# Optimization experiments

Hardware: AMD Instinct MI355X
Metric: run time of the kernel (lower is better)

## Reference

```python
import jax, jax.numpy as jnp
import numpy as np
import math

EMBED_DIM = 512
NUM_HEADS = 8
HEAD_DIM = EMBED_DIM // NUM_HEADS
B, S = 1, 4096


def setup_inputs() -> dict:
    key = jax.random.key(0)
    ks = jax.random.split(key, 9)
    scale = 1.0 / math.sqrt(EMBED_DIM)
    x = jax.random.normal(ks[0], (B, S, EMBED_DIM), dtype=jnp.float32)
    # causal mask, broadcastable to (B, H, S, S); 0 => masked
    mask = jnp.tril(jnp.ones((S, S), dtype=bool))[None, None, :, :]
    Wq = jax.random.normal(ks[1], (EMBED_DIM, EMBED_DIM), jnp.float32) * scale
    bq = jnp.zeros((EMBED_DIM,), jnp.float32)
    Wk = jax.random.normal(ks[2], (EMBED_DIM, EMBED_DIM), jnp.float32) * scale
    bk = jnp.zeros((EMBED_DIM,), jnp.float32)
    Wv = jax.random.normal(ks[3], (EMBED_DIM, EMBED_DIM), jnp.float32) * scale
    bv = jnp.zeros((EMBED_DIM,), jnp.float32)
    Wo = jax.random.normal(ks[4], (EMBED_DIM, EMBED_DIM), jnp.float32) * scale
    bo = jnp.zeros((EMBED_DIM,), jnp.float32)
    return {"x": x, "mask": mask, "Wq": Wq, "bq": bq, "Wk": Wk, "bk": bk,
            "Wv": Wv, "bv": bv, "Wo": Wo, "bo": bo}


def reference(x, mask, Wq, bq, Wk, bk, Wv, bv, Wo, bo):
    Bz, Sz, E = x.shape
    H, D = NUM_HEADS, HEAD_DIM
    qk_scale = math.sqrt(D)
    # linear projections then split heads: (B, S, E) -> (B, H, S, D)
    q = (x @ Wq + bq).reshape(Bz, Sz, H, D).transpose(0, 2, 1, 3)
    k = (x @ Wk + bk).reshape(Bz, Sz, H, D).transpose(0, 2, 1, 3)
    v = (x @ Wv + bv).reshape(Bz, Sz, H, D).transpose(0, 2, 1, 3)
    # naive full score matrix (B, H, S, S) as in the original module
    scores = jnp.einsum('bhqd,bhkd->bhqk', q, k) / qk_scale
    scores = jnp.where(mask, scores, jnp.float32(-jnp.inf))
    attn_weights = jax.nn.softmax(scores, axis=-1)
    attn_output = jnp.einsum('bhqk,bhkd->bhqd', attn_weights, v)
    attn_output = attn_output.transpose(0, 2, 1, 3).reshape(Bz, Sz, E)
    output = attn_output @ Wo + bo
    return output, attn_weights
```

## Files before the change

kernel.cpp:

```cpp
#include <hip/hip_runtime.h>

typedef unsigned short u16;
typedef __attribute__((ext_vector_type(8))) _Float16 f16x8;
typedef __attribute__((ext_vector_type(4))) float f32x4;

#define S 4096
#define E 512
#define NH 8
#define HD 64
#define NG 8
#define KBG 8

__device__ __forceinline__ u16 f2h(float f) {
  union { _Float16 h; u16 u; } v; v.h = (_Float16)f; return v.u;
}

__global__ void xfrag_kernel(const float* __restrict__ x, u16* __restrict__ XF) {
  int o = blockIdx.x * blockDim.x + threadIdx.x;
  int l = o & 63, ks = (o >> 6) & 15, w = (o >> 10) & 3, mb = o >> 12;
  int row = mb * 64 + w * 16 + (l & 15);
  int col = ks * 32 + ((l >> 4) << 3);
  const float4 f0 = *(const float4*)&x[row * 512 + col];
  const float4 f1 = *(const float4*)&x[row * 512 + col + 4];
  f16x8 v;
  v[0] = (_Float16)f0.x; v[1] = (_Float16)f0.y; v[2] = (_Float16)f0.z; v[3] = (_Float16)f0.w;
  v[4] = (_Float16)f1.x; v[5] = (_Float16)f1.y; v[6] = (_Float16)f1.z; v[7] = (_Float16)f1.w;
  *(f16x8*)&XF[o * 8] = v;
}

__global__ void wfrag_kernel(const float* __restrict__ Wq, const float* __restrict__ Wk,
                             const float* __restrict__ Wv, const float* __restrict__ Wo,
                             u16* __restrict__ wqF, u16* __restrict__ wkF,
                             u16* __restrict__ wvF, u16* __restrict__ woF) {
  int o = blockIdx.x * blockDim.x + threadIdx.x;
  int which = blockIdx.y;
  int l = o & 63, ks = (o >> 6) & 15, ct = (o >> 10) & 3, nb = o >> 12;
  int n = nb * 64 + ct * 16 + (l & 15);
  int k0 = ks * 32 + ((l >> 4) << 3);
  const float* W = which == 0 ? Wq : which == 1 ? Wk : which == 2 ? Wv : Wo;
  u16* dst = which == 0 ? wqF : which == 1 ? wkF : which == 2 ? wvF : woF;
  f16x8 v;
#pragma unroll
  for (int j = 0; j < 8; ++j) v[j] = (_Float16)W[(k0 + j) * 512 + n];
  *(f16x8*)&dst[o * 8] = v;
}

template <int MODE>
__global__ __launch_bounds__(256) void gemm_kernel(
    const u16* __restrict__ AF, const u16* __restrict__ BF,
    const float* __restrict__ bias, float premul,
    u16* __restrict__ outh, float* __restrict__ outf) {
  const int mb = blockIdx.x, nb = blockIdx.y;
  const int w = threadIdx.x >> 6, l = threadIdx.x & 63;
  const int lr = l & 15, hi4 = l >> 4;

  f32x4 acc[4] = {{0.f,0.f,0.f,0.f},{0.f,0.f,0.f,0.f},{0.f,0.f,0.f,0.f},{0.f,0.f,0.f,0.f}};

  const u16* abase = AF + (size_t)((mb * 4 + w) * 16) * 512 + l * 8;
  const u16* bbase = BF + (size_t)(nb * 4 * 16) * 512 + l * 8;
#pragma unroll
  for (int ks = 0; ks < 16; ++ks) {
    f16x8 ah = *(const f16x8*)(abase + ks * 512);
#pragma unroll
    for (int ct = 0; ct < 4; ++ct) {
      f16x8 bh = *(const f16x8*)(bbase + (ct * 16 + ks) * 512);
      acc[ct] = __builtin_amdgcn_mfma_f32_16x16x32_f16(ah, bh, acc[ct], 0, 0, 0);
    }
  }

  if constexpr (MODE == 3) {
    __shared__ __align__(16) float sm[4][16][68];
#pragma unroll
    for (int ct = 0; ct < 4; ++ct) {
      float bia = bias[nb * 64 + ct * 16 + lr];
#pragma unroll
      for (int r = 0; r < 4; ++r)
        sm[w][hi4 * 4 + r][ct * 16 + lr] = (acc[ct][r] + bia) * premul;
    }
    asm volatile("s_waitcnt lgkmcnt(0)" ::: "memory");
#pragma unroll
    for (int half = 0; half < 2; ++half) {
      const float* src = &sm[w][lr][half * 32 + hi4 * 8];
      const f32x4 f0 = *(const f32x4*)src;
      const f32x4 f1 = *(const f32x4*)(src + 4);
      f16x8 o8;
      o8[0] = (_Float16)f0[0]; o8[1] = (_Float16)f0[1];
      o8[2] = (_Float16)f0[2]; o8[3] = (_Float16)f0[3];
      o8[4] = (_Float16)f1[0]; o8[5] = (_Float16)f1[1];
      o8[6] = (_Float16)f1[2]; o8[7] = (_Float16)f1[3];
      *(f16x8*)&outh[(size_t)(nb * 64 + mb) * 4096 + w * 1024 + half * 512 + l * 8] = o8;
    }
  } else {
    const int rb = mb * 64 + w * 16 + hi4 * 4;
#pragma unroll
    for (int ct = 0; ct < 4; ++ct) {
      int n = nb * 64 + ct * 16 + lr;
      float bia = bias[n];
#pragma unroll
      for (int r = 0; r < 4; ++r) {
        float v = acc[ct][r] + bia;
        if constexpr (MODE == 0) {
          outh[(rb + r) * E + n] = f2h(v);
        } else {
          outf[(rb + r) * E + n] = v;
        }
      }
    }
  }
}

__global__ void repackV_kernel(const u16* __restrict__ V, u16* __restrict__ VF) {
  int o = blockIdx.x * blockDim.x + threadIdx.x;
  int l = o & 63, half = (o >> 6) & 1, ct = (o >> 7) & 3, kb = (o >> 9) & 63, h = o >> 15;
  int col = h * 64 + ct * 16 + (l & 15);
  int row0 = kb * 64 + half * 32 + ((l >> 4) << 3);
  f16x8 v;
#pragma unroll
  for (int j = 0; j < 8; ++j)
    v[j] = *(const _Float16*)&V[(row0 + j) * 512 + col];
  *(f16x8*)&VF[o * 8] = v;
}

__global__ __launch_bounds__(256) void ksum_kernel(
    const u16* __restrict__ QF, const u16* __restrict__ KF,
    float* __restrict__ ws_l, float* __restrict__ attw) {
  const int gx = blockIdx.x;
  const int h = blockIdx.y;
  const int qb = 63 - (int)blockIdx.z;
  const int kb0 = gx * KBG;
  const int t = threadIdx.x;
  if (kb0 > qb) {
    const size_t base = (size_t)(h * S + qb * 64) * S + gx * 512;
    const f32x4 z = {0.f, 0.f, 0.f, 0.f};
#pragma unroll
    for (int j = 0; j < 32; ++j) {
      int idx = j * 256 + t;
      int row = idx >> 7, c4 = idx & 127;
      __builtin_nontemporal_store(z, (f32x4*)&attw[base + (size_t)row * S + c4 * 4]);
    }
    return;
  }
  const int w = t >> 6, l = t & 63;
  const int lr = l & 15, hi4 = l >> 4;
  const int q0 = qb * 64;

  const int qbase = (h * 64 + qb) * 4096 + w * 1024 + l * 8;
  f16x8 q0f = *(const f16x8*)&QF[qbase];
  f16x8 q1f = *(const f16x8*)&QF[qbase + 512];

  const int rowg = q0 + w * 16 + hi4 * 4;
  float acc[4] = {0.f, 0.f, 0.f, 0.f};

  const int kbend = min(kb0 + KBG, qb + 1);
  for (int kb = kb0; kb < kbend; ++kb) {
    const int kbase = (h * 64 + kb) * 4096 + l * 8;
#pragma unroll
    for (int ct = 0; ct < 4; ++ct) {
      f16x8 k0 = *(const f16x8*)&KF[kbase + ct * 1024];
      f16x8 k1 = *(const f16x8*)&KF[kbase + ct * 1024 + 512];
      f32x4 a = {0.f, 0.f, 0.f, 0.f};
      a = __builtin_amdgcn_mfma_f32_16x16x32_f16(q0f, k0, a, 0, 0, 0);
      a = __builtin_amdgcn_mfma_f32_16x16x32_f16(q1f, k1, a, 0, 0, 0);
      const int colb = kb * 64 + ct * 16 + lr;
#pragma unroll
      for (int r = 0; r < 4; ++r)
        acc[r] += (colb <= rowg + r) ? __expf(a[r]) : 0.f;
    }
  }
#pragma unroll
  for (int r = 0; r < 4; ++r) {
    float v = acc[r];
#pragma unroll
    for (int off = 1; off < 16; off <<= 1) v += __shfl_xor(v, off);
    if (lr == 0) ws_l[(size_t)(h * NG + gx) * S + rowg + r] = v;
  }
}

__global__ void invl_kernel(const float* __restrict__ ws_l, float* __restrict__ invl) {
  int t = blockIdx.x * blockDim.x + threadIdx.x;
  int h = t >> 12, r = t & (S - 1);
  int nc = r >> 9;
  float s = 0.f;
  for (int c = 0; c <= nc; ++c) s += ws_l[(size_t)(h * NG + c) * S + r];
  invl[t] = 1.0f / s;
}

__global__ __launch_bounds__(256) void kwts_kernel(
    const u16* __restrict__ QF, const u16* __restrict__ KF,
    const u16* __restrict__ VF, const float* __restrict__ invl,
    float* __restrict__ attw, u16* __restrict__ ppv) {
  __shared__ __align__(16) float sm[4][16][68];
  const int gx = blockIdx.x;
  const int h = blockIdx.y;
  const int qb = 63 - (int)blockIdx.z;
  const int kb0 = gx * KBG;
  if (kb0 > qb) return;
  const int w = threadIdx.x >> 6, l = threadIdx.x & 63;
  const int lr = l & 15, hi4 = l >> 4, lk = hi4 * 8;
  const int q0 = qb * 64;
  const int rowg = q0 + w * 16 + hi4 * 4;
  const int kbend_c = min(kb0 + KBG, qb + 1);

  const int qbase = (h * 64 + qb) * 4096 + w * 1024 + l * 8;
  f16x8 q0f = *(const f16x8*)&QF[qbase];
  f16x8 q1f = *(const f16x8*)&QF[qbase + 512];
  const float4 iv4 = *(const float4*)&invl[h * S + rowg];
  const float iv[4] = {iv4.x, iv4.y, iv4.z, iv4.w};

  f32x4 o[4] = {{0.f,0.f,0.f,0.f},{0.f,0.f,0.f,0.f},{0.f,0.f,0.f,0.f},{0.f,0.f,0.f,0.f}};

  for (int kb = kb0; kb < kb0 + KBG; ++kb) {
    if (kb < kbend_c) {
      const int kbase = (h * 64 + kb) * 4096 + l * 8;
#pragma unroll
      for (int ct = 0; ct < 4; ++ct) {
        f16x8 k0 = *(const f16x8*)&KF[kbase + ct * 1024];
        f16x8 k1 = *(const f16x8*)&KF[kbase + ct * 1024 + 512];
        f32x4 a = {0.f, 0.f, 0.f, 0.f};
        a = __builtin_amdgcn_mfma_f32_16x16x32_f16(q0f, k0, a, 0, 0, 0);
        a = __builtin_amdgcn_mfma_f32_16x16x32_f16(q1f, k1, a, 0, 0, 0);
        const int colb = kb * 64 + ct * 16 + lr;
#pragma unroll
        for (int r = 0; r < 4; ++r) {
          float pv = (colb <= rowg + r) ? __expf(a[r]) * iv[r] : 0.f;
          sm[w][hi4 * 4 + r][ct * 16 + lr] = pv;
        }
      }
      asm volatile("s_waitcnt lgkmcnt(0)" ::: "memory");
#pragma unroll
      for (int j = 0; j < 4; ++j) {
        const int row16 = hi4 + 4 * j;
        const f32x4 pv4 = *(const f32x4*)&sm[w][row16][lr * 4];
        __builtin_nontemporal_store(
            pv4, (f32x4*)&attw[(size_t)(h * S + q0 + w * 16 + row16) * S + kb * 64 + lr * 4]);
      }
#pragma unroll
      for (int ks = 0; ks < 2; ++ks) {
        const f32x4 f0 = *(const f32x4*)&sm[w][lr][ks * 32 + lk];
        const f32x4 f1 = *(const f32x4*)&sm[w][lr][ks * 32 + lk + 4];
        f16x8 pa;
        pa[0] = (_Float16)f0[0]; pa[1] = (_Float16)f0[1];
        pa[2] = (_Float16)f0[2]; pa[3] = (_Float16)f0[3];
        pa[4] = (_Float16)f1[0]; pa[5] = (_Float16)f1[1];
        pa[6] = (_Float16)f1[2]; pa[7] = (_Float16)f1[3];
        const int vbase = (h * 64 + kb) * 4096 + ks * 512 + l * 8;
#pragma unroll
        for (int ct2 = 0; ct2 < 4; ++ct2) {
          f16x8 bv = *(const f16x8*)&VF[vbase + ct2 * 1024];
          o[ct2] = __builtin_amdgcn_mfma_f32_16x16x32_f16(pa, bv, o[ct2], 0, 0, 0);
        }
      }
      asm volatile("" ::: "memory");
    } else {
      const f32x4 z = {0.f, 0.f, 0.f, 0.f};
#pragma unroll
      for (int j = 0; j < 4; ++j) {
        __builtin_nontemporal_store(
            z, (f32x4*)&attw[(size_t)(h * S + q0 + w * 16 + hi4 + 4 * j) * S + kb * 64 + lr * 4]);
      }
    }
  }

#pragma unroll
  for (int ct2 = 0; ct2 < 4; ++ct2)
#pragma unroll
    for (int r = 0; r < 4; ++r)
      ppv[((size_t)(h * NG + gx) * S + rowg + r) * 64 + ct2 * 16 + lr] = f2h(o[ct2][r]);
}

__global__ void pvred_kernel(const u16* __restrict__ ppv, u16* __restrict__ AOF) {
  int t = blockIdx.x * blockDim.x + threadIdx.x;
  int r = t >> 6, c8 = t & 63;
  int c = c8 * 8;
  int h = c >> 6, dd = c & 63;
  int ng = (r >> 9) + 1;
  float s[8] = {0.f, 0.f, 0.f, 0.f, 0.f, 0.f, 0.f, 0.f};
  for (int g = 0; g < ng; ++g) {
    const f16x8 v = *(const f16x8*)&ppv[((size_t)(h * NG + g) * S + r) * 64 + dd];
#pragma unroll
    for (int j = 0; j < 8; ++j) s[j] += (float)v[j];
  }
  f16x8 o;
#pragma unroll
  for (int j = 0; j < 8; ++j) o[j] = (_Float16)s[j];
  int mb = r >> 6, w = (r >> 4) & 3, ll = r & 15;
  int ks = c >> 5, lhi = (c >> 3) & 3;
  int l = lhi * 16 + ll;
  *(f16x8*)&AOF[(size_t)(((mb * 4 + w) * 16 + ks)) * 512 + l * 8] = o;
}

extern "C" void kernel_launch(void* const* d_in, const int* in_sizes, int n_in,
                              void* d_out, int out_size, void* d_ws, size_t ws_size,
                              hipStream_t stream) {
  const float* x  = (const float*)d_in[0];
  const float* Wq = (const float*)d_in[2];
  const float* bq = (const float*)d_in[3];
  const float* Wk = (const float*)d_in[4];
  const float* bk = (const float*)d_in[5];
  const float* Wv = (const float*)d_in[6];
  const float* bv = (const float*)d_in[7];
  const float* Wo = (const float*)d_in[8];
  const float* bo = (const float*)d_in[9];

  u16* p = (u16*)d_ws;
  u16* XF  = p; p += S * E;
  u16* wqF = p; p += 512 * 512;
  u16* wkF = p; p += 512 * 512;
  u16* wvF = p; p += 512 * 512;
  u16* woF = p; p += 512 * 512;
  u16* QF  = p; p += S * E;
  u16* KF  = p; p += S * E;
  u16* V   = p; p += S * E;
  u16* VF  = p; p += S * E;
  u16* AOF = p; p += S * E;
  size_t ofs = ((size_t)((char*)p - (char*)d_ws) + 15) & ~(size_t)15;
  float* ws_l = (float*)((char*)d_ws + ofs);
  float* invl = ws_l + (size_t)NH * NG * S;
  u16*   ppv  = (u16*)(invl + (size_t)NH * S);
  char* wend = (char*)(ppv + (size_t)NH * NG * S * 64);

  size_t needed = (size_t)(wend - (char*)d_ws);
  if (ws_size < needed) return;

  float* out  = (float*)d_out;
  float* attw = out + (size_t)S * E;

  xfrag_kernel<<<(S * E / 8) / 256, 256, 0, stream>>>(x, XF);
  wfrag_kernel<<<dim3((512 * 512 / 8) / 256, 4), 256, 0, stream>>>(
      Wq, Wk, Wv, Wo, wqF, wkF, wvF, woF);

  dim3 g(S / 64, E / 64);
  gemm_kernel<3><<<g, 256, 0, stream>>>(XF, wqF, bq, 0.125f, QF, nullptr);
  gemm_kernel<3><<<g, 256, 0, stream>>>(XF, wkF, bk, 1.0f, KF, nullptr);
  gemm_kernel<0><<<g, 256, 0, stream>>>(XF, wvF, bv, 1.0f, V, nullptr);

  repackV_kernel<<<(S * E / 8) / 256, 256, 0, stream>>>(V, VF);

  ksum_kernel<<<dim3(NG, NH, S / 64), 256, 0, stream>>>(QF, KF, ws_l, attw);
  invl_kernel<<<(NH * S) / 256, 256, 0, stream>>>(ws_l, invl);
  kwts_kernel<<<dim3(NG, NH, S / 64), 256, 0, stream>>>(QF, KF, VF, invl, attw, ppv);
  pvred_kernel<<<(S * E / 8) / 256, 256, 0, stream>>>(ppv, AOF);

  gemm_kernel<2><<<g, 256, 0, stream>>>(AOF, woF, bo, 1.0f, nullptr, out);
}
```

Baseline: 203.8 us.

## Fuse QKV projections and V repack, fold invl into kwts, use exp2

Merges the three Q/K/V projection GEMMs into one launch with a z grid dimension. The V output is transposed through shared memory straight into the fragment layout, which removes the separate repack kernel and the intermediate V buffer. The inverse row-sum kernel is dropped, and each kwts block now sums the partial row sums itself. Zero-filling of the masked attention-weight tiles moves from ksum to kwts. Q is premultiplied by log2(e)/8 so exp2f replaces __expf, and the per-element causal compare is skipped on off-diagonal tiles; this saves launches and memory traffic at the cost of some redundant row-sum reads.

```diff
diff --git a/kernel.cpp b/kernel.cpp
--- a/kernel.cpp
+++ b/kernel.cpp
@@ -7,9 +7,9 @@
 #define S 4096
 #define E 512
 #define NH 8
-#define HD 64
 #define NG 8
 #define KBG 8
+#define QPREMUL 0.18033688011f
 
 __device__ __forceinline__ u16 f2h(float f) {
   union { _Float16 h; u16 u; } v; v.h = (_Float16)f; return v.u;
@@ -45,19 +45,20 @@
   *(f16x8*)&dst[o * 8] = v;
 }
 
-template <int MODE>
-__global__ __launch_bounds__(256) void gemm_kernel(
-    const u16* __restrict__ AF, const u16* __restrict__ BF,
-    const float* __restrict__ bias, float premul,
-    u16* __restrict__ outh, float* __restrict__ outf) {
-  const int mb = blockIdx.x, nb = blockIdx.y;
+__global__ __launch_bounds__(256) void qkv_kernel(
+    const u16* __restrict__ XF,
+    const u16* __restrict__ wqF, const u16* __restrict__ wkF, const u16* __restrict__ wvF,
+    const float* __restrict__ bq, const float* __restrict__ bk, const float* __restrict__ bv,
+    u16* __restrict__ QF, u16* __restrict__ KF, u16* __restrict__ VF) {
+  const int mb = blockIdx.x, nb = blockIdx.y, z = blockIdx.z;
   const int w = threadIdx.x >> 6, l = threadIdx.x & 63;
   const int lr = l & 15, hi4 = l >> 4;
+  const u16* BF = z == 0 ? wqF : z == 1 ? wkF : wvF;
+  const float* bias = z == 0 ? bq : z == 1 ? bk : bv;
 
   f32x4 acc[4] = {{0.f,0.f,0.f,0.f},{0.f,0.f,0.f,0.f},{0.f,0.f,0.f,0.f},{0.f,0.f,0.f,0.f}};
-
-  const u16* abase = AF + (size_t)((mb * 4 + w) * 16) * 512 + l * 8;
-  const u16* bbase = BF + (size_t)(nb * 4 * 16) * 512 + l * 8;
+  const u16* abase = XF + (size_t)((mb * 4 + w) * 16) * 512 + l * 8;
+  const u16* bbase = BF + (size_t)(nb * 64) * 512 + l * 8;
 #pragma unroll
   for (int ks = 0; ks < 16; ++ks) {
     f16x8 ah = *(const f16x8*)(abase + ks * 512);
@@ -68,8 +69,10 @@
     }
   }
 
-  if constexpr (MODE == 3) {
-    __shared__ __align__(16) float sm[4][16][68];
+  __shared__ __align__(16) char smraw[64 * 69 * 4];
+  if (z < 2) {
+    float (*sm)[16][68] = (float (*)[16][68])smraw;
+    const float premul = z == 0 ? QPREMUL : 1.0f;
 #pragma unroll
     for (int ct = 0; ct < 4; ++ct) {
       float bia = bias[nb * 64 + ct * 16 + lr];
@@ -78,6 +81,7 @@
         sm[w][hi4 * 4 + r][ct * 16 + lr] = (acc[ct][r] + bia) * premul;
     }
     asm volatile("s_waitcnt lgkmcnt(0)" ::: "memory");
+    u16* dst = z == 0 ? QF : KF;
 #pragma unroll
     for (int half = 0; half < 2; ++half) {
       const float* src = &sm[w][lr][half * 32 + hi4 * 8];
@@ -88,59 +92,38 @@
       o8[2] = (_Float16)f0[2]; o8[3] = (_Float16)f0[3];
       o8[4] = (_Float16)f1[0]; o8[5] = (_Float16)f1[1];
       o8[6] = (_Float16)f1[2]; o8[7] = (_Float16)f1[3];
-      *(f16x8*)&outh[(size_t)(nb * 64 + mb) * 4096 + w * 1024 + half * 512 + l * 8] = o8;
+      *(f16x8*)&dst[(size_t)(nb * 64 + mb) * 4096 + w * 1024 + half * 512 + l * 8] = o8;
     }
   } else {
-    const int rb = mb * 64 + w * 16 + hi4 * 4;
-#pragma unroll
-    for (int ct = 0; ct < 4; ++ct) {
-      int n = nb * 64 + ct * 16 + lr;
-      float bia = bias[n];
-#pragma unroll
-      for (int r = 0; r < 4; ++r) {
-        float v = acc[ct][r] + bia;
-        if constexpr (MODE == 0) {
-          outh[(rb + r) * E + n] = f2h(v);
-        } else {
-          outf[(rb + r) * E + n] = v;
-        }
-      }
-    }
-  }
-}
-
-__global__ void repackV_kernel(const u16* __restrict__ V, u16* __restrict__ VF) {
-  int o = blockIdx.x * blockDim.x + threadIdx.x;
-  int l = o & 63, half = (o >> 6) & 1, ct = (o >> 7) & 3, kb = (o >> 9) & 63, h = o >> 15;
-  int col = h * 64 + ct * 16 + (l & 15);
-  int row0 = kb * 64 + half * 32 + ((l >> 4) << 3);
-  f16x8 v;
-#pragma unroll
-  for (int j = 0; j < 8; ++j)
-    v[j] = *(const _Float16*)&V[(row0 + j) * 512 + col];
-  *(f16x8*)&VF[o * 8] = v;
+    float (*sm)[69] = (float (*)[69])smraw;
+#pragma unroll
+    for (int ct = 0; ct < 4; ++ct) {
+      float bia = bias[nb * 64 + ct * 16 + lr];
+#pragma unroll
+      for (int r = 0; r < 4; ++r)
+        sm[w * 16 + hi4 * 4 + r][ct * 16 + lr] = acc[ct][r] + bia;
+    }
+    __syncthreads();
+#pragma unroll
+    for (int hh = 0; hh < 2; ++hh) {
+      f16x8 v;
+#pragma unroll
+      for (int j = 0; j < 8; ++j)
+        v[j] = (_Float16)sm[hh * 32 + hi4 * 8 + j][w * 16 + lr];
+      *(f16x8*)&VF[(size_t)(nb * 64 + mb) * 4096 + w * 1024 + hh * 512 + l * 8] = v;
+    }
+  }
 }
 
 __global__ __launch_bounds__(256) void ksum_kernel(
     const u16* __restrict__ QF, const u16* __restrict__ KF,
-    float* __restrict__ ws_l, float* __restrict__ attw) {
+    float* __restrict__ ws_l) {
   const int gx = blockIdx.x;
   const int h = blockIdx.y;
   const int qb = 63 - (int)blockIdx.z;
   const int kb0 = gx * KBG;
-  const int t = threadIdx.x;
-  if (kb0 > qb) {
-    const size_t base = (size_t)(h * S + qb * 64) * S + gx * 512;
-    const f32x4 z = {0.f, 0.f, 0.f, 0.f};
-#pragma unroll
-    for (int j = 0; j < 32; ++j) {
-      int idx = j * 256 + t;
-      int row = idx >> 7, c4 = idx & 127;
-      __builtin_nontemporal_store(z, (f32x4*)&attw[base + (size_t)row * S + c4 * 4]);
-    }
-    return;
-  }
-  const int w = t >> 6, l = t & 63;
+  if (kb0 > qb) return;
+  const int w = threadIdx.x >> 6, l = threadIdx.x & 63;
   const int lr = l & 15, hi4 = l >> 4;
   const int q0 = qb * 64;
 
@@ -161,10 +144,15 @@
       f32x4 a = {0.f, 0.f, 0.f, 0.f};
       a = __builtin_amdgcn_mfma_f32_16x16x32_f16(q0f, k0, a, 0, 0, 0);
       a = __builtin_amdgcn_mfma_f32_16x16x32_f16(q1f, k1, a, 0, 0, 0);
-      const int colb = kb * 64 + ct * 16 + lr;
-#pragma unroll
-      for (int r = 0; r < 4; ++r)
-        acc[r] += (colb <= rowg + r) ? __expf(a[r]) : 0.f;
+      if (kb != qb) {
+#pragma unroll
+        for (int r = 0; r < 4; ++r) acc[r] += exp2f(a[r]);
+      } else {
+        const int colb = kb * 64 + ct * 16 + lr;
+#pragma unroll
+        for (int r = 0; r < 4; ++r)
+          acc[r] += (colb <= rowg + r) ? exp2f(a[r]) : 0.f;
+      }
     }
   }
 #pragma unroll
@@ -176,36 +164,47 @@
   }
 }
 
-__global__ void invl_kernel(const float* __restrict__ ws_l, float* __restrict__ invl) {
-  int t = blockIdx.x * blockDim.x + threadIdx.x;
-  int h = t >> 12, r = t & (S - 1);
-  int nc = r >> 9;
-  float s = 0.f;
-  for (int c = 0; c <= nc; ++c) s += ws_l[(size_t)(h * NG + c) * S + r];
-  invl[t] = 1.0f / s;
-}
-
 __global__ __launch_bounds__(256) void kwts_kernel(
     const u16* __restrict__ QF, const u16* __restrict__ KF,
-    const u16* __restrict__ VF, const float* __restrict__ invl,
+    const u16* __restrict__ VF, const float* __restrict__ ws_l,
     float* __restrict__ attw, u16* __restrict__ ppv) {
   __shared__ __align__(16) float sm[4][16][68];
   const int gx = blockIdx.x;
   const int h = blockIdx.y;
   const int qb = 63 - (int)blockIdx.z;
   const int kb0 = gx * KBG;
-  if (kb0 > qb) return;
-  const int w = threadIdx.x >> 6, l = threadIdx.x & 63;
+  const int t = threadIdx.x;
+  const int q0 = qb * 64;
+
+  if (kb0 > qb) {
+    const size_t base = (size_t)(h * S + q0) * S + gx * 512;
+    const f32x4 z = {0.f, 0.f, 0.f, 0.f};
+#pragma unroll
+    for (int j = 0; j < 32; ++j) {
+      int idx = j * 256 + t;
+      int row = idx >> 7, c4 = idx & 127;
+      __builtin_nontemporal_store(z, (f32x4*)&attw[base + (size_t)row * S + c4 * 4]);
+    }
+    return;
+  }
+
+  const int w = t >> 6, l = t & 63;
   const int lr = l & 15, hi4 = l >> 4, lk = hi4 * 8;
-  const int q0 = qb * 64;
   const int rowg = q0 + w * 16 + hi4 * 4;
   const int kbend_c = min(kb0 + KBG, qb + 1);
 
   const int qbase = (h * 64 + qb) * 4096 + w * 1024 + l * 8;
   f16x8 q0f = *(const f16x8*)&QF[qbase];
   f16x8 q1f = *(const f16x8*)&QF[qbase + 512];
-  const float4 iv4 = *(const float4*)&invl[h * S + rowg];
-  const float iv[4] = {iv4.x, iv4.y, iv4.z, iv4.w};
+
+  const int ngc = (qb >> 3) + 1;
+  float iv[4];
+#pragma unroll
+  for (int r = 0; r < 4; ++r) {
+    float ssum = 0.f;
+    for (int c = 0; c < ngc; ++c) ssum += ws_l[(size_t)(h * NG + c) * S + rowg + r];
+    iv[r] = 1.0f / ssum;
+  }
 
   f32x4 o[4] = {{0.f,0.f,0.f,0.f},{0.f,0.f,0.f,0.f},{0.f,0.f,0.f,0.f},{0.f,0.f,0.f,0.f}};
 
@@ -219,11 +218,16 @@
         f32x4 a = {0.f, 0.f, 0.f, 0.f};
         a = __builtin_amdgcn_mfma_f32_16x16x32_f16(q0f, k0, a, 0, 0, 0);
         a = __builtin_amdgcn_mfma_f32_16x16x32_f16(q1f, k1, a, 0, 0, 0);
-        const int colb = kb * 64 + ct * 16 + lr;
-#pragma unroll
-        for (int r = 0; r < 4; ++r) {
-          float pv = (colb <= rowg + r) ? __expf(a[r]) * iv[r] : 0.f;
-          sm[w][hi4 * 4 + r][ct * 16 + lr] = pv;
+        if (kb != qb) {
+#pragma unroll
+          for (int r = 0; r < 4; ++r)
+            sm[w][hi4 * 4 + r][ct * 16 + lr] = exp2f(a[r]) * iv[r];
+        } else {
+          const int colb = kb * 64 + ct * 16 + lr;
+#pragma unroll
+          for (int r = 0; r < 4; ++r)
+            sm[w][hi4 * 4 + r][ct * 16 + lr] =
+                (colb <= rowg + r) ? exp2f(a[r]) * iv[r] : 0.f;
         }
       }
       asm volatile("s_waitcnt lgkmcnt(0)" ::: "memory");
@@ -287,6 +291,36 @@
   int ks = c >> 5, lhi = (c >> 3) & 3;
   int l = lhi * 16 + ll;
   *(f16x8*)&AOF[(size_t)(((mb * 4 + w) * 16 + ks)) * 512 + l * 8] = o;
+}
+
+__global__ __launch_bounds__(256) void gemm_o_kernel(
+    const u16* __restrict__ AF, const u16* __restrict__ BF,
+    const float* __restrict__ bias, float* __restrict__ outf) {
+  const int mb = blockIdx.x, nb = blockIdx.y;
+  const int w = threadIdx.x >> 6, l = threadIdx.x & 63;
+  const int lr = l & 15, hi4 = l >> 4;
+
+  f32x4 acc[4] = {{0.f,0.f,0.f,0.f},{0.f,0.f,0.f,0.f},{0.f,0.f,0.f,0.f},{0.f,0.f,0.f,0.f}};
+  const u16* abase = AF + (size_t)((mb * 4 + w) * 16) * 512 + l * 8;
+  const u16* bbase = BF + (size_t)(nb * 64) * 512 + l * 8;
+#pragma unroll
+  for (int ks = 0; ks < 16; ++ks) {
+    f16x8 ah = *(const f16x8*)(abase + ks * 512);
+#pragma unroll
+    for (int ct = 0; ct < 4; ++ct) {
+      f16x8 bh = *(const f16x8*)(bbase + (ct * 16 + ks) * 512);
+      acc[ct] = __builtin_amdgcn_mfma_f32_16x16x32_f16(ah, bh, acc[ct], 0, 0, 0);
+    }
+  }
+  const int rb = mb * 64 + w * 16 + hi4 * 4;
+#pragma unroll
+  for (int ct = 0; ct < 4; ++ct) {
+    int n = nb * 64 + ct * 16 + lr;
+    float bia = bias[n];
+#pragma unroll
+    for (int r = 0; r < 4; ++r)
+      outf[(rb + r) * E + n] = acc[ct][r] + bia;
+  }
 }
 
 extern "C" void kernel_launch(void* const* d_in, const int* in_sizes, int n_in,
@@ -310,13 +344,11 @@
   u16* woF = p; p += 512 * 512;
   u16* QF  = p; p += S * E;
   u16* KF  = p; p += S * E;
-  u16* V   = p; p += S * E;
   u16* VF  = p; p += S * E;
   u16* AOF = p; p += S * E;
   size_t ofs = ((size_t)((char*)p - (char*)d_ws) + 15) & ~(size_t)15;
   float* ws_l = (float*)((char*)d_ws + ofs);
-  float* invl = ws_l + (size_t)NH * NG * S;
-  u16*   ppv  = (u16*)(invl + (size_t)NH * S);
+  u16*   ppv  = (u16*)(ws_l + (size_t)NH * NG * S);
   char* wend = (char*)(ppv + (size_t)NH * NG * S * 64);
 
   size_t needed = (size_t)(wend - (char*)d_ws);
@@ -329,17 +361,12 @@
   wfrag_kernel<<<dim3((512 * 512 / 8) / 256, 4), 256, 0, stream>>>(
       Wq, Wk, Wv, Wo, wqF, wkF, wvF, woF);
 
-  dim3 g(S / 64, E / 64);
-  gemm_kernel<3><<<g, 256, 0, stream>>>(XF, wqF, bq, 0.125f, QF, nullptr);
-  gemm_kernel<3><<<g, 256, 0, stream>>>(XF, wkF, bk, 1.0f, KF, nullptr);
-  gemm_kernel<0><<<g, 256, 0, stream>>>(XF, wvF, bv, 1.0f, V, nullptr);
-
-  repackV_kernel<<<(S * E / 8) / 256, 256, 0, stream>>>(V, VF);
-
-  ksum_kernel<<<dim3(NG, NH, S / 64), 256, 0, stream>>>(QF, KF, ws_l, attw);
-  invl_kernel<<<(NH * S) / 256, 256, 0, stream>>>(ws_l, invl);
-  kwts_kernel<<<dim3(NG, NH, S / 64), 256, 0, stream>>>(QF, KF, VF, invl, attw, ppv);
+  qkv_kernel<<<dim3(S / 64, E / 64, 3), 256, 0, stream>>>(
+      XF, wqF, wkF, wvF, bq, bk, bv, QF, KF, VF);
+
+  ksum_kernel<<<dim3(NG, NH, S / 64), 256, 0, stream>>>(QF, KF, ws_l);
+  kwts_kernel<<<dim3(NG, NH, S / 64), 256, 0, stream>>>(QF, KF, VF, ws_l, attw, ppv);
   pvred_kernel<<<(S * E / 8) / 256, 256, 0, stream>>>(ppv, AOF);
 
-  gemm_kernel<2><<<g, 256, 0, stream>>>(AOF, woF, bo, 1.0f, nullptr, out);
-}
+  gemm_o_kernel<<<dim3(S / 64, E / 64), 256, 0, stream>>>(AOF, woF, bo, out);
+}
```

Measured after the change: 192.3 us, median of 2. -5.7%, faster.
